# Kernel tuning notes

Measured on AMD Instinct MI355X. Metric: run time of the kernel, lower is better.

The kernel has to match this reference:

```python
import jax, jax.numpy as jnp
import numpy as np
from jax import lax

B, CIN, VS, P, E, H = 1, 1, 64, 4, 64, 8
N = (VS // P) ** 3  # 4096 patches
OUT = CIN * P ** 3  # 64
SCALE = 1.0 / float(np.sqrt(E))
EPS = 1e-5


def setup_inputs() -> dict:
    key = jax.random.key(0)
    ks = jax.random.split(key, 8)
    sc = 0.02
    return {
        "voxel": jax.random.normal(ks[0], (B, CIN, VS, VS, VS), jnp.float32),
        "conv_w": jax.random.normal(ks[1], (E, CIN, P, P, P), jnp.float32) * sc,
        "conv_b": jnp.zeros((E,), jnp.float32),
        "ln_g": jnp.ones((E,), jnp.float32),
        "ln_b": jnp.zeros((E,), jnp.float32),
        "pos_emb": jax.random.normal(ks[2], (1, N, E), jnp.float32) * sc,
        "wqk": jax.random.normal(ks[3], (E, H * E), jnp.float32) * sc,
        "bqk": jnp.zeros((H * E,), jnp.float32),
        "wv": jax.random.normal(ks[4], (E, H * E), jnp.float32) * sc,
        "bv": jnp.zeros((H * E,), jnp.float32),
        "alpha": jnp.array(1.0, jnp.float32),
        "wout": jax.random.normal(ks[5], (H * E, OUT), jnp.float32) * sc,
        "bout": jnp.zeros((OUT,), jnp.float32),
    }


def reference(voxel, conv_w, conv_b, ln_g, ln_b, pos_emb, wqk, bqk, wv, bv, alpha, wout, bout):
    # VoxelPatchEmbedding: strided Conv3d -> flatten -> permute -> LayerNorm
    emb = lax.conv_general_dilated(
        voxel, conv_w, window_strides=(P, P, P), padding="VALID",
        dimension_numbers=("NCDHW", "OIDHW", "NCDHW"))
    emb = emb + conv_b[None, :, None, None, None]
    b = emb.shape[0]
    emb = emb.reshape(b, E, -1).transpose(0, 2, 1)  # [B, N, E]
    mu = jnp.mean(emb, axis=-1, keepdims=True)
    var = jnp.var(emb, axis=-1, keepdims=True)
    emb = (emb - mu) * lax.rsqrt(var + EPS) * ln_g + ln_b
    emb = emb + pos_emb

    # tied Q/K projection; heads to dim 1: [B, H, N, E]
    qk_proj = (emb @ wqk + bqk).reshape(b, -1, H, E).transpose(0, 2, 1, 3)
    q = qk_proj
    k = qk_proj
    v = (emb @ wv + bv).reshape(b, -1, H, E).transpose(0, 2, 1, 3)

    # L2 distance: q^2 + k^2 - 2 q.k^T  -> [B, H, N, N]
    q2 = jnp.sum(q * q, axis=-1, keepdims=True)           # [B,H,N,1]
    k2 = jnp.sum(k * k, axis=-1, keepdims=True)           # [B,H,N,1]
    dist = q2 + k2.transpose(0, 1, 3, 2) - 2.0 * jnp.einsum("bhnd,bhmd->bhnm", q, k)

    scores = alpha * jnp.exp(-dist) * SCALE
    attn_w = jax.nn.softmax(scores, axis=-1)
    attn = jnp.einsum("bhnm,bhmd->bhnd", attn_w, v)       # [B,H,N,E]
    attn = attn.transpose(0, 2, 1, 3).reshape(b, -1, H * E)
    return attn @ wout + bout                              # [B, N, CIN*P^3]
```

## Files before the change

kernel.cpp:

```cpp
#include <hip/hip_runtime.h>
#include <hip/hip_bf16.h>

#define NPAT 4096
#define EDIM 64
#define NH   8
#define HE   512
#define OUTD 64

typedef short bf16x8 __attribute__((ext_vector_type(8)));
typedef float f32x4  __attribute__((ext_vector_type(4)));

#if __has_builtin(__builtin_amdgcn_exp2f)
#define EXP2(x) __builtin_amdgcn_exp2f(x)
#else
#define EXP2(x) exp2f(x)
#endif

__device__ __forceinline__ ushort f2bf(float f) {
    uint u = __builtin_bit_cast(uint, f);
    return (ushort)((u + 0x7FFFu + ((u >> 16) & 1u)) >> 16);
}
__device__ __forceinline__ float bf2f(ushort b) {
    return __builtin_bit_cast(float, ((uint)b) << 16);
}

__global__ __launch_bounds__(256) void k_embed(
    const float* __restrict__ voxel,
    const float* __restrict__ conv_w,
    const float* __restrict__ conv_b,
    const float* __restrict__ ln_g, const float* __restrict__ ln_b,
    const float* __restrict__ pos,
    float* __restrict__ emb)
{
    const int b = blockIdx.x;
    const int d = b >> 4, hh = b & 15;
    const int t = threadIdx.x;
    __shared__ float wsm[64][65];
    __shared__ float vox[16][64];

    for (int i = t; i < 4096; i += 256) wsm[i >> 6][i & 63] = conv_w[i];
    {
        const int pair = t >> 4;
        const int off4 = (t & 15) * 4;
        const float4 v = *(const float4*)&voxel[(d * 4 + (pair >> 2)) * 4096 +
                                                (hh * 4 + (pair & 3)) * 64 + off4];
        *(float4*)&vox[pair][off4] = v;
    }
    __syncthreads();

    const int wv = t >> 6;
    const int l  = t & 63;
    const int p  = wv * 4 + (l >> 4);
    const int eb = l & 15;
    const int n  = b * 16 + p;

    float acc[4];
    #pragma unroll
    for (int o = 0; o < 4; o++) acc[o] = conv_b[eb + 16 * o];
    for (int m = 0; m < 64; m++) {
        const float v = vox[m >> 2][p * 4 + (m & 3)];
        #pragma unroll
        for (int o = 0; o < 4; o++) acc[o] += v * wsm[eb + 16 * o][m];
    }

    float s1 = acc[0] + acc[1] + acc[2] + acc[3];
    float s2 = acc[0] * acc[0] + acc[1] * acc[1] + acc[2] * acc[2] + acc[3] * acc[3];
    #pragma unroll
    for (int off = 1; off < 16; off <<= 1) {
        s1 += __shfl_xor(s1, off);
        s2 += __shfl_xor(s2, off);
    }
    const float mu  = s1 * (1.0f / 64.0f);
    const float var = s2 * (1.0f / 64.0f) - mu * mu;
    const float rs  = rsqrtf(var + 1e-5f);
    #pragma unroll
    for (int o = 0; o < 4; o++) {
        const int e = eb + 16 * o;
        emb[n * 64 + e] = (acc[o] - mu) * rs * ln_g[e] + ln_b[e] + pos[n * 64 + e];
    }
}

__global__ __launch_bounds__(256) void k_wt(
    const float* __restrict__ wout,
    ushort* __restrict__ woutT)
{
    const int b = blockIdx.x;
    const int t = threadIdx.x;
    __shared__ float ld[64][65];
    for (int i = t; i < 4096; i += 256) ld[i >> 6][i & 63] = wout[(b * 64 + (i >> 6)) * 64 + (i & 63)];
    __syncthreads();
    const int o = t >> 2, kb = (t & 3) * 16;
    #pragma unroll
    for (int j = 0; j < 16; j++)
        woutT[o * 512 + b * 64 + kb + j] = f2bf(ld[kb + j][o]);
}

__global__ __launch_bounds__(256) void k_proj(
    const float* __restrict__ emb,
    const float* __restrict__ wqk, const float* __restrict__ bqk,
    const float* __restrict__ wv,  const float* __restrict__ bvv,
    ushort* __restrict__ qk_bf,
    ushort* __restrict__ vT_bf)
{
    const int n0 = blockIdx.x * 16;
    const int t = threadIdx.x;
    __shared__ float es[16][64];
    for (int i = t; i < 16 * 64; i += 256) es[i >> 6][i & 63] = emb[n0 * 64 + i];
    __syncthreads();

    const int he0 = t, he1 = t + 256;
    const float bq0 = bqk[he0], bq1 = bqk[he1];
    const float bv0 = bvv[he0], bv1 = bvv[he1];

    for (int rc = 0; rc < 2; rc++) {
        float aq0[8], aq1[8], av0[8], av1[8];
        #pragma unroll
        for (int r = 0; r < 8; r++) { aq0[r] = bq0; aq1[r] = bq1; av0[r] = bv0; av1[r] = bv1; }
        for (int e = 0; e < 64; e++) {
            const float wq0 = wqk[e * HE + he0], wq1 = wqk[e * HE + he1];
            const float wv0 = wv [e * HE + he0], wv1 = wv [e * HE + he1];
            #pragma unroll
            for (int r = 0; r < 8; r++) {
                const float x = es[rc * 8 + r][e];
                aq0[r] += x * wq0; aq1[r] += x * wq1;
                av0[r] += x * wv0; av1[r] += x * wv1;
            }
        }
        #pragma unroll
        for (int r = 0; r < 8; r++) {
            const int n = n0 + rc * 8 + r;
            qk_bf[((he0 >> 6) * NPAT + n) * 64 + (he0 & 63)] = f2bf(aq0[r]);
            qk_bf[((he1 >> 6) * NPAT + n) * 64 + (he1 & 63)] = f2bf(aq1[r]);
            vT_bf[((he0 >> 6) * 64 + (he0 & 63)) * NPAT + n] = f2bf(av0[r]);
            vT_bf[((he1 >> 6) * 64 + (he1 & 63)) * NPAT + n] = f2bf(av1[r]);
        }
    }
}

__global__ __launch_bounds__(256) void k_q2(
    const ushort* __restrict__ qk_bf, float* __restrict__ q2)
{
    const int i = blockIdx.x * 256 + threadIdx.x;
    const ushort* row = qk_bf + (size_t)i * 64;
    float s = 0.0f;
    #pragma unroll
    for (int c = 0; c < 8; c++) {
        bf16x8 v = *(const bf16x8*)(row + c * 8);
        #pragma unroll
        for (int j = 0; j < 8; j++) { float f = bf2f((ushort)v[j]); s += f * f; }
    }
    q2[i] = s;
}

__global__ __launch_bounds__(1024, 8) void k_attn(
    const ushort* __restrict__ qk,
    const ushort* __restrict__ vT,
    const float* __restrict__ q2,
    const float* __restrict__ alpha,
    ushort* __restrict__ attn)
{
    const int bid = blockIdx.x;
    const int h  = bid & 7;
    const int bx = bid >> 3;
    const int tid = threadIdx.x;
    const int w  = tid >> 6;
    const int u  = w & 3;
    const int rg = w >> 2;
    const int l  = tid & 63;
    const int lr = l & 15;
    const int lg = l >> 4;
    const float L2E = 1.4426950408889634f;
    const float ccl2e = alpha[0] * 0.125f * L2E;

    __shared__ ushort kv_lds[2][2][64 * 64];
    __shared__ ushort p_lds[4][16 * 64];
    __shared__ float  zpart[4][4][16];

    const ushort* qkh = qk + (size_t)h * NPAT * 64;
    const ushort* vTh = vT + (size_t)h * 64 * NPAT;
    const float*  q2h = q2 + h * NPAT;

    const int row0 = bx * 64 + rg * 16;

    bf16x8 aq0, aq1;
    {
        const ushort* qrow = qkh + (size_t)(row0 + lr) * 64 + 8 * lg;
        aq0 = *(const bf16x8*)(qrow);
        aq1 = *(const bf16x8*)(qrow + 32);
    }
    float nq2[4];
    #pragma unroll
    for (int r = 0; r < 4; r++) nq2[r] = q2h[row0 + 4 * lg + r];

    const int w8   = w & 7;
    const int srow = w8 * 8 + (l >> 3);
    const int sch  = (l & 7) ^ (srow & 7);
    const ushort* ksrc0 = qkh + (size_t)srow * 64 + sch * 8;
    const ushort* vsrc0 = vTh + (size_t)srow * NPAT + sch * 8;
#define STAGE(bufi, it)                                                          \
    do {                                                                         \
        const ushort* _src = (w < 8) ? (ksrc0 + (size_t)(it) * 4096)             \
                                     : (vsrc0 + (size_t)(it) * 64);              \
        ushort* _dst = &kv_lds[bufi][w >> 3][w8 * 512];                          \
        __builtin_amdgcn_global_load_lds(                                        \
            (const __attribute__((address_space(1))) unsigned int*)_src,         \
            (__attribute__((address_space(3))) unsigned int*)_dst, 16, 0, 0);    \
    } while (0)

    f32x4 acc = (f32x4){0.f, 0.f, 0.f, 0.f};
    float zacc[4] = {0.f, 0.f, 0.f, 0.f};

    const int x7 = (lr & 7);
    char* prg = (char*)&p_lds[rg][0];

    STAGE(0, 0);
    float k2c = q2h[u * 16 + lr];

    for (int it = 0; it < 64; ++it) {
        const int buf = it & 1;
        __syncthreads();
        if (it + 1 < 64) STAGE(buf ^ 1, it + 1);
        float k2n = (it + 1 < 64) ? q2h[(it + 1) * 64 + u * 16 + lr] : 0.f;

        {
            const ushort* kb = &kv_lds[buf][0][0];
            const int krow = u * 16 + lr;
            bf16x8 bk0 = *(const bf16x8*)(kb + krow * 64 + ((lg ^ x7) << 3));
            bf16x8 bk1 = *(const bf16x8*)(kb + krow * 64 + (((lg + 4) ^ x7) << 3));
            f32x4 sc = (f32x4){0.f, 0.f, 0.f, 0.f};
            sc = __builtin_amdgcn_mfma_f32_16x16x32_bf16(aq0, bk0, sc, 0, 0, 0);
            sc = __builtin_amdgcn_mfma_f32_16x16x32_bf16(aq1, bk1, sc, 0, 0, 0);
            #pragma unroll
            for (int r = 0; r < 4; r++) {
                const float d = nq2[r] + k2c - 2.0f * sc[r];
                const float p = EXP2(ccl2e * EXP2(-L2E * d));
                zacc[r] += p;
                const int prow = 4 * lg + r, pcol = 16 * u + lr;
                const int byteoff = prow * 128 + ((pcol * 2) ^ ((prow & 7) << 4));
                *(ushort*)(prg + byteoff) = f2bf(p);
            }
        }
        asm volatile("s_waitcnt lgkmcnt(0)" ::: "memory");
        __builtin_amdgcn_s_barrier();

        {
            const ushort* vb = &kv_lds[buf][1][0];
            const int vrow = u * 16 + lr;
            bf16x8 bv0 = *(const bf16x8*)(vb + vrow * 64 + ((lg ^ x7) << 3));
            bf16x8 bv1 = *(const bf16x8*)(vb + vrow * 64 + (((lg + 4) ^ x7) << 3));
            char* rb = prg + lr * 128;
            const int xx = x7 << 4;
            bf16x8 pa0 = *(const bf16x8*)(rb + ((16 * lg) ^ xx));
            bf16x8 pa1 = *(const bf16x8*)(rb + ((64 + 16 * lg) ^ xx));
            acc = __builtin_amdgcn_mfma_f32_16x16x32_bf16(pa0, bv0, acc, 0, 0, 0);
            acc = __builtin_amdgcn_mfma_f32_16x16x32_bf16(pa1, bv1, acc, 0, 0, 0);
        }
        k2c = k2n;
    }
#undef STAGE

    #pragma unroll
    for (int r = 0; r < 4; r++) {
        float z = zacc[r];
        z += __shfl_xor(z, 1); z += __shfl_xor(z, 2);
        z += __shfl_xor(z, 4); z += __shfl_xor(z, 8);
        if (lr == 0) zpart[rg][u][4 * lg + r] = z;
    }
    __syncthreads();
    #pragma unroll
    for (int r = 0; r < 4; r++) {
        const int row = 4 * lg + r;
        const float zt = zpart[rg][0][row] + zpart[rg][1][row] +
                         zpart[rg][2][row] + zpart[rg][3][row];
        attn[(size_t)(row0 + row) * HE + h * 64 + u * 16 + lr] = f2bf(acc[r] / zt);
    }
}

__global__ __launch_bounds__(256) void k_out(
    const ushort* __restrict__ attn,
    const ushort* __restrict__ woutT,
    const float* __restrict__ bout,
    float* __restrict__ out)
{
    const int n0 = blockIdx.x * 16;
    const int t = threadIdx.x;
    const int w = t >> 6, l = t & 63, lr = l & 15, lg = l >> 4;
    __shared__ ushort sa[16][520];

    for (int c = t; c < 1024; c += 256) {
        const int row = c >> 6, c8 = c & 63;
        *(bf16x8*)&sa[row][c8 * 8] = *(const bf16x8*)&attn[(size_t)(n0 + row) * 512 + c8 * 8];
    }
    __syncthreads();

    f32x4 acc = (f32x4){0.f, 0.f, 0.f, 0.f};
    const ushort* bp = woutT + (size_t)(w * 16 + lr) * 512 + 8 * lg;
    #pragma unroll
    for (int kk = 0; kk < 16; kk++) {
        bf16x8 a = *(const bf16x8*)&sa[lr][kk * 32 + 8 * lg];
        bf16x8 bb = *(const bf16x8*)(bp + kk * 32);
        acc = __builtin_amdgcn_mfma_f32_16x16x32_bf16(a, bb, acc, 0, 0, 0);
    }
    const float bo = bout[w * 16 + lr];
    #pragma unroll
    for (int r = 0; r < 4; r++)
        out[(size_t)(n0 + 4 * lg + r) * 64 + w * 16 + lr] = acc[r] + bo;
}

extern "C" void kernel_launch(void* const* d_in, const int* in_sizes, int n_in,
                              void* d_out, int out_size, void* d_ws, size_t ws_size,
                              hipStream_t stream) {
    (void)in_sizes; (void)n_in; (void)out_size; (void)ws_size;
    const float* voxel  = (const float*)d_in[0];
    const float* conv_w = (const float*)d_in[1];
    const float* conv_b = (const float*)d_in[2];
    const float* ln_g   = (const float*)d_in[3];
    const float* ln_b   = (const float*)d_in[4];
    const float* pos    = (const float*)d_in[5];
    const float* wqk    = (const float*)d_in[6];
    const float* bqk    = (const float*)d_in[7];
    const float* wv     = (const float*)d_in[8];
    const float* bvv    = (const float*)d_in[9];
    const float* alpha  = (const float*)d_in[10];
    const float* wout   = (const float*)d_in[11];
    const float* bout   = (const float*)d_in[12];
    float* out = (float*)d_out;

    char* ws = (char*)d_ws;
    float*  emb     = (float*) (ws);
    ushort* qk_bf   = (ushort*)(ws + (1u << 20));
    ushort* vT_bf   = (ushort*)(ws + 5u * (1u << 20));
    float*  q2      = (float*) (ws + 9u * (1u << 20));
    ushort* attn_bf = (ushort*)(ws + 9u * (1u << 20) + (128u << 10));
    ushort* woutT   = (ushort*)(ws + 13u * (1u << 20) + (128u << 10));

    k_embed<<<256, 256, 0, stream>>>(voxel, conv_w, conv_b, ln_g, ln_b, pos, emb);
    k_wt<<<8, 256, 0, stream>>>(wout, woutT);
    k_proj<<<NPAT / 16, 256, 0, stream>>>(emb, wqk, bqk, wv, bvv, qk_bf, vT_bf);
    k_q2<<<(NH * NPAT) / 256, 256, 0, stream>>>(qk_bf, q2);
    k_attn<<<NPAT / 64 * NH, 1024, 0, stream>>>(qk_bf, vT_bf, q2, alpha, attn_bf);
    k_out<<<NPAT / 16, 256, 0, stream>>>(attn_bf, woutT, bout, out);
}
```

Before: 203.9 us.

## Widen grids for embed/proj/out kernels and fuse q2 into projection

```diff
diff --git a/kernel.cpp b/kernel.cpp
--- a/kernel.cpp
+++ b/kernel.cpp
@@ -9,6 +9,7 @@
 
 typedef short bf16x8 __attribute__((ext_vector_type(8)));
 typedef float f32x4  __attribute__((ext_vector_type(4)));
+typedef unsigned short u16x4 __attribute__((ext_vector_type(4)));
 
 #if __has_builtin(__builtin_amdgcn_exp2f)
 #define EXP2(x) __builtin_amdgcn_exp2f(x)
@@ -33,51 +34,42 @@
     float* __restrict__ emb)
 {
     const int b = blockIdx.x;
-    const int d = b >> 4, hh = b & 15;
+    const int d = b >> 6, hh = (b >> 2) & 15, wq = b & 3;
     const int t = threadIdx.x;
-    __shared__ float wsm[64][65];
-    __shared__ float vox[16][64];
+    __shared__ float wsm[64][68];
+    __shared__ float vox[4][64];
 
     for (int i = t; i < 4096; i += 256) wsm[i >> 6][i & 63] = conv_w[i];
     {
         const int pair = t >> 4;
-        const int off4 = (t & 15) * 4;
-        const float4 v = *(const float4*)&voxel[(d * 4 + (pair >> 2)) * 4096 +
-                                                (hh * 4 + (pair & 3)) * 64 + off4];
-        *(float4*)&vox[pair][off4] = v;
-    }
-    __syncthreads();
-
-    const int wv = t >> 6;
-    const int l  = t & 63;
-    const int p  = wv * 4 + (l >> 4);
-    const int eb = l & 15;
-    const int n  = b * 16 + p;
-
-    float acc[4];
-    #pragma unroll
-    for (int o = 0; o < 4; o++) acc[o] = conv_b[eb + 16 * o];
-    for (int m = 0; m < 64; m++) {
-        const float v = vox[m >> 2][p * 4 + (m & 3)];
-        #pragma unroll
-        for (int o = 0; o < 4; o++) acc[o] += v * wsm[eb + 16 * o][m];
-    }
-
-    float s1 = acc[0] + acc[1] + acc[2] + acc[3];
-    float s2 = acc[0] * acc[0] + acc[1] * acc[1] + acc[2] * acc[2] + acc[3] * acc[3];
-    #pragma unroll
-    for (int off = 1; off < 16; off <<= 1) {
+        const int q16  = t & 15;
+        const float v = voxel[(d * 4 + (pair >> 2)) * 4096 + (hh * 4 + (pair & 3)) * 64 +
+                              wq * 16 + q16];
+        vox[q16 >> 2][pair * 4 + (q16 & 3)] = v;
+    }
+    __syncthreads();
+
+    const int p = t >> 6;
+    const int e = t & 63;
+    const int n = d * 256 + hh * 16 + wq * 4 + p;
+
+    float acc = conv_b[e];
+    #pragma unroll
+    for (int mi = 0; mi < 16; mi++) {
+        const float4 vv = *(const float4*)&vox[p][mi * 4];
+        const float4 ww = *(const float4*)&wsm[e][mi * 4];
+        acc += vv.x * ww.x + vv.y * ww.y + vv.z * ww.z + vv.w * ww.w;
+    }
+
+    float s1 = acc, s2 = acc * acc;
+    #pragma unroll
+    for (int off = 1; off < 64; off <<= 1) {
         s1 += __shfl_xor(s1, off);
         s2 += __shfl_xor(s2, off);
     }
     const float mu  = s1 * (1.0f / 64.0f);
     const float var = s2 * (1.0f / 64.0f) - mu * mu;
-    const float rs  = rsqrtf(var + 1e-5f);
-    #pragma unroll
-    for (int o = 0; o < 4; o++) {
-        const int e = eb + 16 * o;
-        emb[n * 64 + e] = (acc[o] - mu) * rs * ln_g[e] + ln_b[e] + pos[n * 64 + e];
-    }
+    emb[n * 64 + e] = (acc - mu) * rsqrtf(var + 1e-5f) * ln_g[e] + ln_b[e] + pos[n * 64 + e];
 }
 
 __global__ __launch_bounds__(256) void k_wt(
@@ -100,56 +92,47 @@
     const float* __restrict__ wqk, const float* __restrict__ bqk,
     const float* __restrict__ wv,  const float* __restrict__ bvv,
     ushort* __restrict__ qk_bf,
-    ushort* __restrict__ vT_bf)
+    ushort* __restrict__ vT_bf,
+    float* __restrict__ q2)
 {
     const int n0 = blockIdx.x * 16;
-    const int t = threadIdx.x;
+    const int h  = blockIdx.y;
+    const int t  = threadIdx.x;
+    const int e  = t & 63, rg = t >> 6;
     __shared__ float es[16][64];
-    for (int i = t; i < 16 * 64; i += 256) es[i >> 6][i & 63] = emb[n0 * 64 + i];
-    __syncthreads();
-
-    const int he0 = t, he1 = t + 256;
-    const float bq0 = bqk[he0], bq1 = bqk[he1];
-    const float bv0 = bvv[he0], bv1 = bvv[he1];
-
-    for (int rc = 0; rc < 2; rc++) {
-        float aq0[8], aq1[8], av0[8], av1[8];
+    for (int i = t; i < 1024; i += 256) es[i >> 6][i & 63] = emb[n0 * 64 + i];
+    __syncthreads();
+
+    const int he = h * 64 + e;
+    const float bq = bqk[he], bv = bvv[he];
+    float aq[4] = {bq, bq, bq, bq};
+    float av[4] = {bv, bv, bv, bv};
+
+    for (int ep = 0; ep < 64; ep++) {
+        const float wq = wqk[ep * HE + he];
+        const float wvv = wv[ep * HE + he];
         #pragma unroll
-        for (int r = 0; r < 8; r++) { aq0[r] = bq0; aq1[r] = bq1; av0[r] = bv0; av1[r] = bv1; }
-        for (int e = 0; e < 64; e++) {
-            const float wq0 = wqk[e * HE + he0], wq1 = wqk[e * HE + he1];
-            const float wv0 = wv [e * HE + he0], wv1 = wv [e * HE + he1];
-            #pragma unroll
-            for (int r = 0; r < 8; r++) {
-                const float x = es[rc * 8 + r][e];
-                aq0[r] += x * wq0; aq1[r] += x * wq1;
-                av0[r] += x * wv0; av1[r] += x * wv1;
-            }
+        for (int rr = 0; rr < 4; rr++) {
+            const float x = es[rg * 4 + rr][ep];
+            aq[rr] += x * wq;
+            av[rr] += x * wvv;
         }
+    }
+
+    u16x4 vpk;
+    #pragma unroll
+    for (int rr = 0; rr < 4; rr++) {
+        const int n = n0 + rg * 4 + rr;
+        const ushort qb = f2bf(aq[rr]);
+        qk_bf[((size_t)h * NPAT + n) * 64 + e] = qb;
+        const float qf = bf2f(qb);
+        float s = qf * qf;
         #pragma unroll
-        for (int r = 0; r < 8; r++) {
-            const int n = n0 + rc * 8 + r;
-            qk_bf[((he0 >> 6) * NPAT + n) * 64 + (he0 & 63)] = f2bf(aq0[r]);
-            qk_bf[((he1 >> 6) * NPAT + n) * 64 + (he1 & 63)] = f2bf(aq1[r]);
-            vT_bf[((he0 >> 6) * 64 + (he0 & 63)) * NPAT + n] = f2bf(av0[r]);
-            vT_bf[((he1 >> 6) * 64 + (he1 & 63)) * NPAT + n] = f2bf(av1[r]);
-        }
-    }
-}
-
-__global__ __launch_bounds__(256) void k_q2(
-    const ushort* __restrict__ qk_bf, float* __restrict__ q2)
-{
-    const int i = blockIdx.x * 256 + threadIdx.x;
-    const ushort* row = qk_bf + (size_t)i * 64;
-    float s = 0.0f;
-    #pragma unroll
-    for (int c = 0; c < 8; c++) {
-        bf16x8 v = *(const bf16x8*)(row + c * 8);
-        #pragma unroll
-        for (int j = 0; j < 8; j++) { float f = bf2f((ushort)v[j]); s += f * f; }
-    }
-    q2[i] = s;
+        for (int off = 1; off < 64; off <<= 1) s += __shfl_xor(s, off);
+        if (e == 0) q2[h * NPAT + n] = s;
+        vpk[rr] = f2bf(av[rr]);
+    }
+    *(u16x4*)&vT_bf[((size_t)h * 64 + e) * NPAT + n0 + rg * 4] = vpk;
 }
 
 __global__ __launch_bounds__(1024, 8) void k_attn(
@@ -282,12 +265,12 @@
     const float* __restrict__ bout,
     float* __restrict__ out)
 {
-    const int n0 = blockIdx.x * 16;
+    const int n0 = blockIdx.x * 8;
     const int t = threadIdx.x;
     const int w = t >> 6, l = t & 63, lr = l & 15, lg = l >> 4;
-    __shared__ ushort sa[16][520];
-
-    for (int c = t; c < 1024; c += 256) {
+    __shared__ ushort sa[8][520];
+
+    for (int c = t; c < 512; c += 256) {
         const int row = c >> 6, c8 = c & 63;
         *(bf16x8*)&sa[row][c8 * 8] = *(const bf16x8*)&attn[(size_t)(n0 + row) * 512 + c8 * 8];
     }
@@ -297,14 +280,16 @@
     const ushort* bp = woutT + (size_t)(w * 16 + lr) * 512 + 8 * lg;
     #pragma unroll
     for (int kk = 0; kk < 16; kk++) {
-        bf16x8 a = *(const bf16x8*)&sa[lr][kk * 32 + 8 * lg];
+        bf16x8 a = *(const bf16x8*)&sa[lr & 7][kk * 32 + 8 * lg];
         bf16x8 bb = *(const bf16x8*)(bp + kk * 32);
         acc = __builtin_amdgcn_mfma_f32_16x16x32_bf16(a, bb, acc, 0, 0, 0);
     }
-    const float bo = bout[w * 16 + lr];
-    #pragma unroll
-    for (int r = 0; r < 4; r++)
-        out[(size_t)(n0 + 4 * lg + r) * 64 + w * 16 + lr] = acc[r] + bo;
+    if (lg < 2) {
+        const float bo = bout[w * 16 + lr];
+        #pragma unroll
+        for (int r = 0; r < 4; r++)
+            out[(size_t)(n0 + 4 * lg + r) * 64 + w * 16 + lr] = acc[r] + bo;
+    }
 }
 
 extern "C" void kernel_launch(void* const* d_in, const int* in_sizes, int n_in,
@@ -334,10 +319,9 @@
     ushort* attn_bf = (ushort*)(ws + 9u * (1u << 20) + (128u << 10));
     ushort* woutT   = (ushort*)(ws + 13u * (1u << 20) + (128u << 10));
 
-    k_embed<<<256, 256, 0, stream>>>(voxel, conv_w, conv_b, ln_g, ln_b, pos, emb);
+    k_embed<<<1024, 256, 0, stream>>>(voxel, conv_w, conv_b, ln_g, ln_b, pos, emb);
     k_wt<<<8, 256, 0, stream>>>(wout, woutT);
-    k_proj<<<NPAT / 16, 256, 0, stream>>>(emb, wqk, bqk, wv, bvv, qk_bf, vT_bf);
-    k_q2<<<(NH * NPAT) / 256, 256, 0, stream>>>(qk_bf, q2);
+    k_proj<<<dim3(NPAT / 16, NH), 256, 0, stream>>>(emb, wqk, bqk, wv, bvv, qk_bf, vT_bf, q2);
     k_attn<<<NPAT / 64 * NH, 1024, 0, stream>>>(qk_bf, vT_bf, q2, alpha, attn_bf);
-    k_out<<<NPAT / 16, 256, 0, stream>>>(attn_bf, woutT, bout, out);
-}
+    k_out<<<NPAT / 8, 256, 0, stream>>>(attn_bf, woutT, bout, out);
+}
```

Result: no change. 202.1 us (-0.9%).
